# Kernel tuning notes

Hardware: AMD Instinct MI355X
Metric: run time of the kernel (lower is better)

The kernel has to match this reference:

```python
import jax, jax.numpy as jnp
import numpy as np

# Bit-slice configuration from the module defaults: slices [1,1,2,4] -> 8-bit signed INT.
# The crossbar engine's MapReduceDot decomposes the quantized integers into bit-planes,
# runs partial dot products per (input-slice, weight-slice) pair across paral_size
# partitions, and recombines them with 2^shift weights. In the ideal (noise-free)
# engine this recombination is EXACT, so the forward math equals:
#   dequant(blockwise_quant(x)) @ dequant(blockwise_quant(W^T)) + bias
# with per-block scales determined by the quant granularities.
IN_BITS = 1 + 1 + 2 + 4   # sum(input_slice)  = 8
W_BITS = 1 + 1 + 2 + 4    # sum(weight_slice) = 8
IN_GRAN = (1, 32)         # (rows, cols) blocks over (seq, in_features)
W_GRAN = (32, 32)         # blocks over (in_features, out_features) of weight.t()


def block_fake_quant(x, bits, gran):
    """Symmetric per-block fake quantization (quantize -> dequantize).

    x: [..., R, C]; gran=(gr, gc) tiles the last two dims. Each (gr, gc) block
    gets its own max-abs scale, matching SlicedData's quant_gran semantics.
    """
    qmax = float(2 ** (bits - 1) - 1)  # 127 for 8-bit
    gr, gc = gran
    lead = x.shape[:-2]
    R, C = x.shape[-2], x.shape[-1]
    xb = x.reshape(*lead, R // gr, gr, C // gc, gc)
    mx = jnp.max(jnp.abs(xb), axis=(-3, -1), keepdims=True)
    scale = jnp.where(mx > 0, mx / qmax, jnp.ones_like(mx))
    q = jnp.clip(jnp.round(xb / scale), -qmax, qmax) * scale
    return q.reshape(x.shape)


def setup_inputs() -> dict:
    key = jax.random.key(0)
    k1, k2, k3 = jax.random.split(key, 3)
    B, S, Din, Dout = 4, 4096, 2048, 2048
    x = jax.random.normal(k1, (B, S, Din), dtype=jnp.float32)
    # kaiming_uniform_(a=sqrt(5)) on a Linear weight is U(-1/sqrt(fan_in), 1/sqrt(fan_in))
    bound = 1.0 / np.sqrt(Din)
    weight = jax.random.uniform(k2, (Dout, Din), jnp.float32, -bound, bound)
    bias = jax.random.uniform(k3, (Dout,), jnp.float32, -bound, bound)
    return {"x": x, "weight": weight, "bias": bias}


def reference(x, weight, bias):
    # Quantize activations per (1, 32) block and weight.t() per (32, 32) block,
    # then recombine via the (mathematically exact) bit-sliced dot == dense GEMM
    # on the dequantized values.
    qx = block_fake_quant(x, IN_BITS, IN_GRAN)            # [B, S, Din]
    qw = block_fake_quant(weight.T, W_BITS, W_GRAN)       # [Din, Dout]
    out = jnp.einsum('bsd,de->bse', qx, qw) + bias        # [B, S, Dout]
    return out
```

## Files before the change

kernel.cpp:

```cpp
#include <hip/hip_runtime.h>
#include <hip/hip_bf16.h>
#include <stdint.h>

#define M_TOT 16384
#define N_TOT 2048
#define K_TOT 2048
#define NT 32
#define QW_BLOCKS 1024

typedef __attribute__((ext_vector_type(8))) short bf16x8;
typedef __attribute__((ext_vector_type(4))) float f32x4;

__device__ __forceinline__ ushort f32_to_bf16_rne(float f) {
    uint32_t u = __float_as_uint(f);
    uint32_t r = (u + 0x7fffu + ((u >> 16) & 1u)) >> 16;
    return (ushort)r;
}

__device__ __forceinline__ void async_copy16(const void* gptr, void* lptr) {
    __builtin_amdgcn_global_load_lds(
        (const __attribute__((address_space(1))) uint32_t*)gptr,
        (__attribute__((address_space(3))) uint32_t*)lptr,
        16, 0, 0);
}

__global__ void quant_fused_kernel(const float* __restrict__ x,
                                   const float* __restrict__ w,
                                   ushort* __restrict__ qx,
                                   ushort* __restrict__ qw) {
    if (blockIdx.x < QW_BLOCKS) {
        const int gtid = blockIdx.x * 256 + threadIdx.x;
        const int wid  = gtid >> 6;
        const int lane = gtid & 63;
        const int tn = wid >> 6;
        const int tk = wid & 63;
        const int row = tn * 32 + (lane >> 1);
        const int col = tk * 32 + ((lane & 1) << 4);
        const float* p = w + (size_t)row * K_TOT + col;
        const float4 v0 = ((const float4*)p)[0];
        const float4 v1 = ((const float4*)p)[1];
        const float4 v2 = ((const float4*)p)[2];
        const float4 v3 = ((const float4*)p)[3];
        float m = 0.f;
#define MAX4(V) m = fmaxf(m, fmaxf(fmaxf(fabsf(V.x), fabsf(V.y)), fmaxf(fabsf(V.z), fabsf(V.w))));
        MAX4(v0) MAX4(v1) MAX4(v2) MAX4(v3)
#undef MAX4
        #pragma unroll
        for (int off = 1; off < 64; off <<= 1) m = fmaxf(m, __shfl_xor(m, off));
        const float s = (m > 0.f) ? (m / 127.f) : 1.f;
        float vv[16] = {v0.x, v0.y, v0.z, v0.w, v1.x, v1.y, v1.z, v1.w,
                        v2.x, v2.y, v2.z, v2.w, v3.x, v3.y, v3.z, v3.w};
        union { ushort us[16]; uint4 q[2]; } o;
        #pragma unroll
        for (int i = 0; i < 16; ++i) {
            const float q = fminf(fmaxf(rintf(vv[i] / s), -127.f), 127.f) * s;
            o.us[i] = f32_to_bf16_rne(q);
        }
        uint4* dst = (uint4*)(qw + (size_t)row * K_TOT + col);
        dst[0] = o.q[0];
        dst[1] = o.q[1];
    } else {
        const int tid = (blockIdx.x - QW_BLOCKS) * 256 + threadIdx.x;
        const float4 v = ((const float4*)x)[tid];
        float m = fmaxf(fmaxf(fabsf(v.x), fabsf(v.y)), fmaxf(fabsf(v.z), fabsf(v.w)));
        m = fmaxf(m, __shfl_xor(m, 1));
        m = fmaxf(m, __shfl_xor(m, 2));
        m = fmaxf(m, __shfl_xor(m, 4));
        const float s = (m > 0.f) ? (m / 127.f) : 1.f;
        const float q0 = fminf(fmaxf(rintf(v.x / s), -127.f), 127.f) * s;
        const float q1 = fminf(fmaxf(rintf(v.y / s), -127.f), 127.f) * s;
        const float q2 = fminf(fmaxf(rintf(v.z / s), -127.f), 127.f) * s;
        const float q3 = fminf(fmaxf(rintf(v.w / s), -127.f), 127.f) * s;
        ushort4 r;
        r.x = f32_to_bf16_rne(q0);
        r.y = f32_to_bf16_rne(q1);
        r.z = f32_to_bf16_rne(q2);
        r.w = f32_to_bf16_rne(q3);
        ((ushort4*)qx)[tid] = r;
    }
}

#define LDSA(tb, row, colus) \
    (*(const bf16x8*)&As[tb][row][(colus) ^ (((row) & 7) << 3)])
#define LDSB(slot, row, colus) \
    (*(const bf16x8*)&Bs[slot][row][(colus) ^ (((row) & 7) << 3)])

#define STAGE_A(tb, hh, li, tt)                                                          \
    async_copy16(Agbase + (size_t)((hh) * 128 + (li) * 64) * K_TOT + (size_t)(tt) * 64,  \
                 (char*)&As[0][0][0] + (tb) * 32768 + (hh) * 16384 + (li) * 8192 + (wv << 10));
#define STAGE_B(slot, hh, li, tt)                                                        \
    async_copy16(Bgbase + (size_t)((hh) * 128 + (li) * 64) * K_TOT + (size_t)(tt) * 64,  \
                 (char*)&Bs[0][0][0] + (size_t)(slot) * 32768 + (hh) * 16384 + (li) * 8192 + (wv << 10));
#define STAGE_A2(tb, hh, tt)    { STAGE_A(tb, hh, 0, tt) STAGE_A(tb, hh, 1, tt) }
#define STAGE_B2(slot, hh, tt)  { STAGE_B(slot, hh, 0, tt) STAGE_B(slot, hh, 1, tt) }

#define WAITLGKM4 { asm volatile("s_waitcnt lgkmcnt(4)" ::: "memory"); __builtin_amdgcn_sched_barrier(0); }
#define WAITLGKM0 { asm volatile("s_waitcnt lgkmcnt(0)" ::: "memory"); __builtin_amdgcn_sched_barrier(0); }

#define RD_AF(DST, tb, q) {                                   \
    DST[0] = LDSA(tb, ab + (q) * 32,      h8);                \
    DST[1] = LDSA(tb, ab + (q) * 32,      32 + h8);           \
    DST[2] = LDSA(tb, ab + (q) * 32 + 16, h8);                \
    DST[3] = LDSA(tb, ab + (q) * 32 + 16, 32 + h8); }

#define RD_BG(slot) {                                                         \
    _Pragma("unroll")                                                         \
    for (int j = 0; j < 4; ++j) {                                             \
        const int bb = wcn * 64 + j * 16 + r;                                 \
        bg[j][0] = LDSB(slot, bb, h8);  bg[j][1] = LDSB(slot, bb, 32 + h8);   \
    } }

#define MFMA_PH(i0, AF)                                                                   \
    __builtin_amdgcn_s_setprio(1);                                                        \
    _Pragma("unroll")                                                                     \
    for (int j = 0; j < 4; ++j) {                                                         \
        acc[i0][j]     = __builtin_amdgcn_mfma_f32_16x16x32_bf16(AF[0], bg[j][0], acc[i0][j], 0, 0, 0);     \
        acc[i0][j]     = __builtin_amdgcn_mfma_f32_16x16x32_bf16(AF[1], bg[j][1], acc[i0][j], 0, 0, 0);     \
        acc[(i0)+1][j] = __builtin_amdgcn_mfma_f32_16x16x32_bf16(AF[2], bg[j][0], acc[(i0)+1][j], 0, 0, 0); \
        acc[(i0)+1][j] = __builtin_amdgcn_mfma_f32_16x16x32_bf16(AF[3], bg[j][1], acc[(i0)+1][j], 0, 0, 0); \
    }                                                                                     \
    __builtin_amdgcn_s_setprio(0);

#define TILE_BODY(tb, t, STA, STB, VMC, BRD, BWR)                                         \
  {                                                                                       \
                   \
    RD_AF(afX, tb, 0)                                                                     \
    RD_BG(BRD)                                                                            \
    RD_AF(afY, tb, 1)                                                                     \
    if (STA) STAGE_A2(tb ^ 1, 0, (t) + 1)                                                 \
    WAITLGKM4                                                                             \
    MFMA_PH(0, afX)                                                                       \
                                        \
    RD_AF(afX, tb, 2)                                                                     \
    if (STA) STAGE_A2(tb ^ 1, 1, (t) + 1)                                                 \
    WAITLGKM4                                                                             \
    MFMA_PH(2, afY)                                                                       \
                     \
    RD_AF(afY, tb, 3)                                                                     \
    if (STB) STAGE_B2(BWR, 0, (t) + 2)                                                    \
    WAITLGKM4                                                                             \
    MFMA_PH(4, afX)                                                                       \
                    \
    if (STB) STAGE_B2(BWR, 1, (t) + 2)                                                    \
    WAITLGKM0                                                                             \
    MFMA_PH(6, afY)                                                                       \
    if ((VMC) == 4)      { asm volatile("s_waitcnt vmcnt(4)" ::: "memory"); }             \
    else if ((VMC) == 0) { asm volatile("s_waitcnt vmcnt(0)" ::: "memory"); }             \
    __builtin_amdgcn_s_barrier();          \
  }

__global__ __launch_bounds__(512, 2) void gemm_pipe5_kernel(
    const ushort* __restrict__ A,
    const ushort* __restrict__ Bt,
    const float* __restrict__ bias,
    float* __restrict__ C) {

    __shared__ ushort As[2][256][64];
    __shared__ ushort Bs[3][256][64];

    const int tid  = threadIdx.x;
    const int lane = tid & 63;
    const int wv   = tid >> 6;
    const int wmr  = wv >> 2;
    const int wcn  = wv & 3;
    const int r    = lane & 15;
    const int h8   = (lane >> 4) << 3;

    const int nbn  = N_TOT / 256;
    const int nwg  = (M_TOT / 256) * nbn;
    const int cpx  = nwg >> 3;
    const int swz  = (blockIdx.x & 7) * cpx + (blockIdx.x >> 3);
    const int brow = (swz / nbn) * 256;
    const int bcol = (swz % nbn) * 256;

    const int srow = tid >> 3;
    const int scol = (((tid & 7) ^ (srow & 7)) << 3);
    const ushort* Agbase = A  + (size_t)(brow + srow) * K_TOT + scol;
    const ushort* Bgbase = Bt + (size_t)(bcol + srow) * K_TOT + scol;

    const int ab = wmr * 128 + r;

    f32x4 acc[8][4];
    const f32x4 zero = {0.f, 0.f, 0.f, 0.f};
    #pragma unroll
    for (int i = 0; i < 8; ++i)
        #pragma unroll
        for (int j = 0; j < 4; ++j) acc[i][j] = zero;

    STAGE_A2(0, 0, 0) STAGE_A2(0, 1, 0)
    STAGE_B2(0, 0, 0) STAGE_B2(0, 1, 0)
    STAGE_B2(1, 0, 1) STAGE_B2(1, 1, 1)
    asm volatile("s_waitcnt vmcnt(4)" ::: "memory");
    __builtin_amdgcn_s_barrier();

    bf16x8 afX[4], afY[4];
    bf16x8 bg[4][2];

    int brd = 0;
    int bwr = 2;

    for (int t = 0; t < NT - 2; t += 2) {
        TILE_BODY(0, t,     1, 1, 4, brd, bwr)
        brd = (brd == 2) ? 0 : brd + 1;  bwr = (bwr == 2) ? 0 : bwr + 1;
        TILE_BODY(1, t + 1, 1, 1, 4, brd, bwr)
        brd = (brd == 2) ? 0 : brd + 1;  bwr = (bwr == 2) ? 0 : bwr + 1;
    }
    TILE_BODY(0, NT - 2, 1, 0, 0, brd, 0)
    brd = (brd == 2) ? 0 : brd + 1;
    TILE_BODY(1, NT - 1, 0, 0, -1, brd, 0)

    const int hq = (lane >> 4) * 4;
    float bv[4];
    #pragma unroll
    for (int j = 0; j < 4; ++j) bv[j] = bias[bcol + wcn * 64 + j * 16 + r];
    #pragma unroll
    for (int i = 0; i < 8; ++i) {
        const int row0 = brow + wmr * 128 + i * 16 + hq;
        #pragma unroll
        for (int j = 0; j < 4; ++j) {
            const int col = bcol + wcn * 64 + j * 16 + r;
            #pragma unroll
            for (int jj = 0; jj < 4; ++jj)
                C[(size_t)(row0 + jj) * N_TOT + col] = acc[i][j][jj] + bv[j];
        }
    }
}

extern "C" void kernel_launch(void* const* d_in, const int* in_sizes, int n_in,
                              void* d_out, int out_size, void* d_ws, size_t ws_size,
                              hipStream_t stream) {
    const float* x    = (const float*)d_in[0];
    const float* wgt  = (const float*)d_in[1];
    const float* bias = (const float*)d_in[2];
    float* out = (float*)d_out;

    ushort* qx = (ushort*)d_ws;
    ushort* qw = qx + (size_t)M_TOT * K_TOT;

    quant_fused_kernel<<<QW_BLOCKS + (M_TOT * K_TOT / 4) / 256, 256, 0, stream>>>(x, wgt, qx, qw);
    gemm_pipe5_kernel<<<(M_TOT / 256) * (N_TOT / 256), 512, 0, stream>>>(qx, qw, bias, out);
}
```

Baseline: 162.2 us.

## Load B fragments directly from global into registers, dropping B LDS staging

Removes the triple-buffered LDS tile for B. Each wave now loads its B MFMA fragments straight from global memory into double-buffered registers one tile ahead, with vmcnt waits adjusted to match. The block swizzle is replaced by plain row-major block indexing, so the 8 N-column blocks that share an A row tile run next to each other. This cuts LDS footprint and LDS read traffic, but each wave issues uncoalesced 16-byte global loads with no reuse across waves sharing the same columns, and it raises register pressure.

Result: slower. 223.0 us (+37.5%).

```diff
diff --git a/kernel.cpp b/kernel.cpp
--- a/kernel.cpp
+++ b/kernel.cpp
@@ -82,17 +82,11 @@
 
 #define LDSA(tb, row, colus) \
     (*(const bf16x8*)&As[tb][row][(colus) ^ (((row) & 7) << 3)])
-#define LDSB(slot, row, colus) \
-    (*(const bf16x8*)&Bs[slot][row][(colus) ^ (((row) & 7) << 3)])
 
 #define STAGE_A(tb, hh, li, tt)                                                          \
     async_copy16(Agbase + (size_t)((hh) * 128 + (li) * 64) * K_TOT + (size_t)(tt) * 64,  \
                  (char*)&As[0][0][0] + (tb) * 32768 + (hh) * 16384 + (li) * 8192 + (wv << 10));
-#define STAGE_B(slot, hh, li, tt)                                                        \
-    async_copy16(Bgbase + (size_t)((hh) * 128 + (li) * 64) * K_TOT + (size_t)(tt) * 64,  \
-                 (char*)&Bs[0][0][0] + (size_t)(slot) * 32768 + (hh) * 16384 + (li) * 8192 + (wv << 10));
 #define STAGE_A2(tb, hh, tt)    { STAGE_A(tb, hh, 0, tt) STAGE_A(tb, hh, 1, tt) }
-#define STAGE_B2(slot, hh, tt)  { STAGE_B(slot, hh, 0, tt) STAGE_B(slot, hh, 1, tt) }
 
 #define WAITLGKM4 { asm volatile("s_waitcnt lgkmcnt(4)" ::: "memory"); __builtin_amdgcn_sched_barrier(0); }
 #define WAITLGKM0 { asm volatile("s_waitcnt lgkmcnt(0)" ::: "memory"); __builtin_amdgcn_sched_barrier(0); }
@@ -103,60 +97,62 @@
     DST[2] = LDSA(tb, ab + (q) * 32 + 16, h8);                \
     DST[3] = LDSA(tb, ab + (q) * 32 + 16, 32 + h8); }
 
-#define RD_BG(slot) {                                                         \
+#define RD_BGG(DST, tt) {                                                     \
+    const ushort* bp_ = Bgl + (size_t)(tt) * 64;                              \
     _Pragma("unroll")                                                         \
     for (int j = 0; j < 4; ++j) {                                             \
-        const int bb = wcn * 64 + j * 16 + r;                                 \
-        bg[j][0] = LDSB(slot, bb, h8);  bg[j][1] = LDSB(slot, bb, 32 + h8);   \
-    } }
-
-#define MFMA_PH(i0, AF)                                                                   \
+        DST[j][0] = *(const bf16x8*)(bp_ + (size_t)j * (16 * K_TOT));         \
+        DST[j][1] = *(const bf16x8*)(bp_ + (size_t)j * (16 * K_TOT) + 32);    \
+    }                                                                         \
+    __builtin_amdgcn_sched_barrier(0); }
+
+#define MFMA_PH(i0, AF, BGC)                                                              \
     __builtin_amdgcn_s_setprio(1);                                                        \
     _Pragma("unroll")                                                                     \
     for (int j = 0; j < 4; ++j) {                                                         \
-        acc[i0][j]     = __builtin_amdgcn_mfma_f32_16x16x32_bf16(AF[0], bg[j][0], acc[i0][j], 0, 0, 0);     \
-        acc[i0][j]     = __builtin_amdgcn_mfma_f32_16x16x32_bf16(AF[1], bg[j][1], acc[i0][j], 0, 0, 0);     \
-        acc[(i0)+1][j] = __builtin_amdgcn_mfma_f32_16x16x32_bf16(AF[2], bg[j][0], acc[(i0)+1][j], 0, 0, 0); \
-        acc[(i0)+1][j] = __builtin_amdgcn_mfma_f32_16x16x32_bf16(AF[3], bg[j][1], acc[(i0)+1][j], 0, 0, 0); \
+        acc[i0][j]     = __builtin_amdgcn_mfma_f32_16x16x32_bf16(AF[0], BGC[j][0], acc[i0][j], 0, 0, 0);     \
+        acc[i0][j]     = __builtin_amdgcn_mfma_f32_16x16x32_bf16(AF[1], BGC[j][1], acc[i0][j], 0, 0, 0);     \
+        acc[(i0)+1][j] = __builtin_amdgcn_mfma_f32_16x16x32_bf16(AF[2], BGC[j][0], acc[(i0)+1][j], 0, 0, 0); \
+        acc[(i0)+1][j] = __builtin_amdgcn_mfma_f32_16x16x32_bf16(AF[3], BGC[j][1], acc[(i0)+1][j], 0, 0, 0); \
     }                                                                                     \
     __builtin_amdgcn_s_setprio(0);
 
-#define TILE_BODY(tb, t, STA, STB, VMC, BRD, BWR)                                         \
+#define TILE_BODY(tb, t, STA, RDBG, VMP0, VMP3, BGC, BGN)                                 \
   {                                                                                       \
-                   \
+                     \
     RD_AF(afX, tb, 0)                                                                     \
-    RD_BG(BRD)                                                                            \
+    __builtin_amdgcn_sched_barrier(0);              \
     RD_AF(afY, tb, 1)                                                                     \
     if (STA) STAGE_A2(tb ^ 1, 0, (t) + 1)                                                 \
+    if ((VMP0) == 2)      { asm volatile("s_waitcnt vmcnt(2)" ::: "memory"); }            \
+    else if ((VMP0) == 0) { asm volatile("s_waitcnt vmcnt(0)" ::: "memory"); }            \
     WAITLGKM4                                                                             \
-    MFMA_PH(0, afX)                                                                       \
+    MFMA_PH(0, afX, BGC)                                                                  \
                                         \
     RD_AF(afX, tb, 2)                                                                     \
     if (STA) STAGE_A2(tb ^ 1, 1, (t) + 1)                                                 \
     WAITLGKM4                                                                             \
-    MFMA_PH(2, afY)                                                                       \
-                     \
+    MFMA_PH(2, afY, BGC)                                                                  \
+                            \
     RD_AF(afY, tb, 3)                                                                     \
-    if (STB) STAGE_B2(BWR, 0, (t) + 2)                                                    \
+    if (RDBG) RD_BGG(BGN, (t) + 1)                                                        \
     WAITLGKM4                                                                             \
-    MFMA_PH(4, afX)                                                                       \
-                    \
-    if (STB) STAGE_B2(BWR, 1, (t) + 2)                                                    \
+    MFMA_PH(4, afX, BGC)                                                                  \
+           \
     WAITLGKM0                                                                             \
-    MFMA_PH(6, afY)                                                                       \
-    if ((VMC) == 4)      { asm volatile("s_waitcnt vmcnt(4)" ::: "memory"); }             \
-    else if ((VMC) == 0) { asm volatile("s_waitcnt vmcnt(0)" ::: "memory"); }             \
-    __builtin_amdgcn_s_barrier();          \
+    MFMA_PH(6, afY, BGC)                                                                  \
+    if ((VMP3) == 8)      { asm volatile("s_waitcnt vmcnt(8)" ::: "memory"); }            \
+    else if ((VMP3) == 0) { asm volatile("s_waitcnt vmcnt(0)" ::: "memory"); }            \
+    __builtin_amdgcn_s_barrier();                 \
   }
 
-__global__ __launch_bounds__(512, 2) void gemm_pipe5_kernel(
+__global__ __launch_bounds__(512, 2) void gemm_bl2_kernel(
     const ushort* __restrict__ A,
     const ushort* __restrict__ Bt,
     const float* __restrict__ bias,
     float* __restrict__ C) {
 
     __shared__ ushort As[2][256][64];
-    __shared__ ushort Bs[3][256][64];
 
     const int tid  = threadIdx.x;
     const int lane = tid & 63;
@@ -166,17 +162,14 @@
     const int r    = lane & 15;
     const int h8   = (lane >> 4) << 3;
 
-    const int nbn  = N_TOT / 256;
-    const int nwg  = (M_TOT / 256) * nbn;
-    const int cpx  = nwg >> 3;
-    const int swz  = (blockIdx.x & 7) * cpx + (blockIdx.x >> 3);
-    const int brow = (swz / nbn) * 256;
-    const int bcol = (swz % nbn) * 256;
+    const int brow = (blockIdx.x >> 3) * 256;
+    const int bcol = (blockIdx.x & 7) * 256;
 
     const int srow = tid >> 3;
     const int scol = (((tid & 7) ^ (srow & 7)) << 3);
-    const ushort* Agbase = A  + (size_t)(brow + srow) * K_TOT + scol;
-    const ushort* Bgbase = Bt + (size_t)(bcol + srow) * K_TOT + scol;
+    const ushort* Agbase = A + (size_t)(brow + srow) * K_TOT + scol;
+
+    const ushort* Bgl = Bt + (size_t)(bcol + wcn * 64 + r) * K_TOT + h8;
 
     const int ab = wmr * 128 + r;
 
@@ -187,27 +180,20 @@
         #pragma unroll
         for (int j = 0; j < 4; ++j) acc[i][j] = zero;
 
+    bf16x8 afX[4], afY[4];
+    bf16x8 bgA[4][2], bgB[4][2];
+
     STAGE_A2(0, 0, 0) STAGE_A2(0, 1, 0)
-    STAGE_B2(0, 0, 0) STAGE_B2(0, 1, 0)
-    STAGE_B2(1, 0, 1) STAGE_B2(1, 1, 1)
-    asm volatile("s_waitcnt vmcnt(4)" ::: "memory");
+    RD_BGG(bgA, 0)
+    asm volatile("s_waitcnt vmcnt(8)" ::: "memory");
     __builtin_amdgcn_s_barrier();
 
-    bf16x8 afX[4], afY[4];
-    bf16x8 bg[4][2];
-
-    int brd = 0;
-    int bwr = 2;
-
     for (int t = 0; t < NT - 2; t += 2) {
-        TILE_BODY(0, t,     1, 1, 4, brd, bwr)
-        brd = (brd == 2) ? 0 : brd + 1;  bwr = (bwr == 2) ? 0 : bwr + 1;
-        TILE_BODY(1, t + 1, 1, 1, 4, brd, bwr)
-        brd = (brd == 2) ? 0 : brd + 1;  bwr = (bwr == 2) ? 0 : bwr + 1;
+        TILE_BODY(0, t,     1, 1, 2, 8, bgA, bgB)
+        TILE_BODY(1, t + 1, 1, 1, 2, 8, bgB, bgA)
     }
-    TILE_BODY(0, NT - 2, 1, 0, 0, brd, 0)
-    brd = (brd == 2) ? 0 : brd + 1;
-    TILE_BODY(1, NT - 1, 0, 0, -1, brd, 0)
+    TILE_BODY(0, NT - 2, 1, 1, 2, 8, bgA, bgB)
+    TILE_BODY(1, NT - 1, 0, 0, 0, -1, bgB, bgA)
 
     const int hq = (lane >> 4) * 4;
     float bv[4];
@@ -238,5 +224,5 @@
     ushort* qw = qx + (size_t)M_TOT * K_TOT;
 
     quant_fused_kernel<<<QW_BLOCKS + (M_TOT * K_TOT / 4) / 256, 256, 0, stream>>>(x, wgt, qx, qw);
-    gemm_pipe5_kernel<<<(M_TOT / 256) * (N_TOT / 256), 512, 0, stream>>>(qx, qw, bias, out);
-}
+    gemm_bl2_kernel<<<(M_TOT / 256) * (N_TOT / 256), 512, 0, stream>>>(qx, qw, bias, out);
+}
```
